# Kernel optimization log

Hardware: AMD Instinct MI355X
Metric: run time of the kernel (lower is better)

Reference implementation:

```python
import jax, jax.numpy as jnp
import numpy as np


def swish(x):
    return x * jax.nn.sigmoid(x)


def setup_inputs() -> dict:
    key = jax.random.key(0)
    ks = jax.random.split(key, 10)
    N, E, R, H = 50000, 300000, 6, 512
    return {
        "x": jax.random.randint(ks[0], (N,), 0, 95),
        "rbf": jax.random.normal(ks[1], (E, R), dtype=jnp.float32),
        "i": jax.random.randint(ks[2], (E,), 0, N),
        "j": jax.random.randint(ks[3], (E,), 0, N),
        "emb_weight": jax.random.normal(ks[4], (95, H), dtype=jnp.float32),
        "W_rbf0": jax.random.normal(ks[5], (R, H), dtype=jnp.float32) * 0.1,
        "b_rbf0": jax.random.normal(ks[6], (H,), dtype=jnp.float32) * 0.1,
        "W_lin": jax.random.normal(ks[7], (3 * H, H), dtype=jnp.float32) * 0.02,
        "b_lin": jax.random.normal(ks[8], (H,), dtype=jnp.float32) * 0.1,
        "W_rbf1": jax.random.normal(ks[9], (R, H), dtype=jnp.float32) * 0.1,
    }


def reference(x, rbf, i, j, emb_weight, W_rbf0, b_rbf0, W_lin, b_lin, W_rbf1):
    # node embedding lookup: [N, H]
    h = emb_weight[x]
    # radial basis projection + swish: [E, H]
    rbf0 = swish(rbf @ W_rbf0 + b_rbf0)
    # gather endpoints, concat, linear, swish: [E, H]
    cat = jnp.concatenate([h[i], h[j], rbf0], axis=-1)  # [E, 3H]
    e1 = swish(cat @ W_lin + b_lin)
    # bias-free rbf projection, elementwise product: [E, H]
    e2 = (rbf @ W_rbf1) * e1
    return (e1, e2)
```

## Files before the change

### kernel.cpp

```cpp
#include <hip/hip_runtime.h>
#include <hip/hip_bf16.h>

typedef __attribute__((ext_vector_type(8))) short short8;
typedef __attribute__((ext_vector_type(4))) float f32x4;

#define NQ 95
#define HDIM 512
#define RBF 6
#define BM 64

static __device__ __forceinline__ unsigned short f2bf(float f){
  unsigned u = __float_as_uint(f);
  u += 0x7FFF + ((u >> 16) & 1);
  return (unsigned short)(u >> 16);
}
static __device__ __forceinline__ float swishf(float z){
  float e = __expf(-z);
  return z * __builtin_amdgcn_rcpf(1.0f + e);
}

__global__ __launch_bounds__(256) void prep_tables(
    const float* __restrict__ emb, const float* __restrict__ W_lin,
    const float* __restrict__ b_lin, float* __restrict__ P0,
    float* __restrict__ P1)
{
  __shared__ float sE[HDIM];
  const int v   = blockIdx.x % NQ;
  const int tab = blockIdx.x / NQ;
  const int t   = threadIdx.x;
  sE[t]       = emb[v*HDIM + t];
  sE[t + 256] = emb[v*HDIM + t + 256];
  __syncthreads();
  const float* W = W_lin + (size_t)tab * HDIM * HDIM;
  float a0 = tab ? 0.f : b_lin[t];
  float a1 = tab ? 0.f : b_lin[t + 256];
  #pragma unroll 4
  for (int k = 0; k < HDIM; ++k){
    float ew = sE[k];
    a0 += ew * W[(size_t)k*HDIM + t];
    a1 += ew * W[(size_t)k*HDIM + t + 256];
  }
  float* P = tab ? P1 : P0;
  P[v*HDIM + t]       = a0;
  P[v*HDIM + t + 256] = a1;
}

__global__ __launch_bounds__(256) void prep_w2t(
    const float* __restrict__ W_lin, unsigned short* __restrict__ W2T)
{
  const int idx = blockIdx.x * 256 + threadIdx.x;
  const int n  = idx >> 6;
  const int kb = (idx & 63) * 8;
  const float* W2 = W_lin + (size_t)1024 * HDIM;
  unsigned p[4];
  #pragma unroll
  for (int c = 0; c < 4; ++c){
    unsigned lo = f2bf(W2[(size_t)(kb + 2*c    ) * HDIM + n]);
    unsigned hi = f2bf(W2[(size_t)(kb + 2*c + 1) * HDIM + n]);
    p[c] = lo | (hi << 16);
  }
  uint4 o; o.x = p[0]; o.y = p[1]; o.z = p[2]; o.w = p[3];
  *(uint4*)(W2T + (size_t)n * HDIM + kb) = o;
}

__global__ __launch_bounds__(512, 4) void fused_edge(
    const int* __restrict__ xv, const float* __restrict__ rbf,
    const int* __restrict__ ei, const int* __restrict__ ej,
    const float* __restrict__ W0, const float* __restrict__ b0,
    const float* __restrict__ W1,
    const float* __restrict__ P0, const float* __restrict__ P1,
    const unsigned short* __restrict__ W2T,
    float* __restrict__ out, int E)
{
  __shared__ unsigned short sA[BM * HDIM];
  __shared__ float sRbf[BM * RBF];
  __shared__ int sXi[BM], sXj[BM];

  const int t  = threadIdx.x;
  const int eb = blockIdx.x * BM;
  const int me = min(BM, E - eb);

  if (t < 96){
    float4 v = make_float4(0.f, 0.f, 0.f, 0.f);
    size_t gi  = (size_t)eb * RBF + (size_t)t * 4;
    size_t lim = (size_t)E * RBF;
    if (gi + 4 <= lim) v = *(const float4*)(rbf + gi);
    else {
      float* pv = (float*)&v;
      for (int c = 0; c < 4; ++c) if (gi + c < lim) pv[c] = rbf[gi + c];
    }
    *(float4*)(sRbf + t*4) = v;
  } else if (t >= 128 && t < 192){
    int q = t - 128;
    int xi = 0, xj = 0;
    int e = eb + q;
    if (e < E){ xi = xv[ei[e]]; xj = xv[ej[e]]; }
    sXi[q] = xi; sXj[q] = xj;
  }

  const int cp   = t & 255;
  const int half = t >> 8;
  float2 w0c[RBF];
  #pragma unroll
  for (int r = 0; r < RBF; ++r) w0c[r] = *(const float2*)(W0 + r*HDIM + 2*cp);
  float2 bb = *(const float2*)(b0 + 2*cp);

  __syncthreads();

  char* sAb = (char*)sA;
  {
    const int swz_t = 4 * cp;
    const int m0 = half * 32;
    #pragma unroll 2
    for (int mm = 0; mm < 32; ++mm){
      const int m = m0 + mm;
      float2 ra = *(const float2*)(sRbf + m*RBF);
      float2 rb = *(const float2*)(sRbf + m*RBF + 2);
      float2 rc = *(const float2*)(sRbf + m*RBF + 4);
      float z0 = bb.x, z1 = bb.y;
      z0 += ra.x*w0c[0].x + ra.y*w0c[1].x + rb.x*w0c[2].x
          + rb.y*w0c[3].x + rc.x*w0c[4].x + rc.y*w0c[5].x;
      z1 += ra.x*w0c[0].y + ra.y*w0c[1].y + rb.x*w0c[2].y
          + rb.y*w0c[3].y + rc.x*w0c[4].y + rc.y*w0c[5].y;
      unsigned pk = (unsigned)f2bf(swishf(z0)) | ((unsigned)f2bf(swishf(z1)) << 16);
      *(unsigned*)(sAb + (m*1024 + (swz_t ^ ((m & 7) << 4)))) = pk;
    }
  }
  __syncthreads();

  const int lane  = t & 63;
  const int w     = t >> 6;
  const int nbase = w * 64;
  const int rlo   = lane & 15;
  const int kg    = lane >> 4;

  f32x4 acc[4][4];
  #pragma unroll
  for (int a = 0; a < 4; ++a)
    #pragma unroll
    for (int b = 0; b < 4; ++b) acc[a][b] = f32x4{0.f, 0.f, 0.f, 0.f};

  for (int ks = 0; ks < 16; ++ks){
    short8 af[4];
    #pragma unroll
    for (int mt = 0; mt < 4; ++mt){
      int row = mt*16 + rlo;
      int off = row*1024 + ((ks*64 + kg*16) ^ ((row & 7) << 4));
      af[mt] = *(const short8*)(sAb + off);
    }
    short8 bfr[4];
    #pragma unroll
    for (int nt = 0; nt < 4; ++nt){
      int n = nbase + nt*16 + rlo;
      bfr[nt] = *(const short8*)(W2T + (size_t)n*HDIM + ks*32 + kg*8);
    }
    #pragma unroll
    for (int nt = 0; nt < 4; ++nt)
      #pragma unroll
      for (int mt = 0; mt < 4; ++mt)
        acc[mt][nt] = __builtin_amdgcn_mfma_f32_16x16x32_bf16(af[mt], bfr[nt], acc[mt][nt], 0, 0, 0);
  }

  float w1c[RBF][4];
  #pragma unroll
  for (int nt = 0; nt < 4; ++nt){
    int n = nbase + nt*16 + rlo;
    #pragma unroll
    for (int r = 0; r < RBF; ++r) w1c[r][nt] = W1[r*HDIM + n];
  }

  float* __restrict__ out2 = out + (size_t)E * HDIM;
  #pragma unroll
  for (int mt = 0; mt < 4; ++mt){
    #pragma unroll
    for (int r = 0; r < 4; ++r){
      const int m  = mt*16 + kg*4 + r;
      const bool valid = (m < me);
      const int xi = sXi[m], xj = sXj[m];
      const float* p0row = P0 + (size_t)xi * HDIM;
      const float* p1row = P1 + (size_t)xj * HDIM;
      const size_t orow = (size_t)(eb + m) * HDIM;
      float2 rra = *(const float2*)(sRbf + m*RBF);
      float2 rrb = *(const float2*)(sRbf + m*RBF + 2);
      float2 rrc = *(const float2*)(sRbf + m*RBF + 4);
      #pragma unroll
      for (int nt = 0; nt < 4; ++nt){
        const int n = nbase + nt*16 + rlo;
        float f  = acc[mt][nt][r] + p0row[n] + p1row[n];
        float e1 = swishf(f);
        float g  = rra.x*w1c[0][nt] + rra.y*w1c[1][nt] + rrb.x*w1c[2][nt]
                 + rrb.y*w1c[3][nt] + rrc.x*w1c[4][nt] + rrc.y*w1c[5][nt];
        if (valid){
          __builtin_nontemporal_store(e1,    out  + orow + n);
          __builtin_nontemporal_store(g*e1,  out2 + orow + n);
        }
      }
    }
  }
}

extern "C" void kernel_launch(void* const* d_in, const int* in_sizes, int n_in,
                              void* d_out, int out_size, void* d_ws, size_t ws_size,
                              hipStream_t stream) {
  const int*   xv    = (const int*)  d_in[0];
  const float* rbf   = (const float*)d_in[1];
  const int*   ei    = (const int*)  d_in[2];
  const int*   ej    = (const int*)  d_in[3];
  const float* emb   = (const float*)d_in[4];
  const float* W0    = (const float*)d_in[5];
  const float* b0    = (const float*)d_in[6];
  const float* W_lin = (const float*)d_in[7];
  const float* b_lin = (const float*)d_in[8];
  const float* W1    = (const float*)d_in[9];
  float* out = (float*)d_out;

  const int E = in_sizes[2];

  float* P0 = (float*)d_ws;
  float* P1 = P0 + NQ * HDIM;
  unsigned short* W2T = (unsigned short*)(P1 + NQ * HDIM);

  prep_tables<<<2 * NQ, 256, 0, stream>>>(emb, W_lin, b_lin, P0, P1);
  prep_w2t<<<(HDIM * (HDIM/8)) / 256, 256, 0, stream>>>(W_lin, W2T);

  const int nblk = (E + BM - 1) / BM;
  fused_edge<<<nblk, 512, 0, stream>>>(xv, rbf, ei, ej, W0, b0, W1,
                                       P0, P1, W2T, out, E);
}
```

Before: 537.4 us.

## Double thread count per block in fused edge and prep kernels

The fused edge kernel now launches 1024 threads (16 waves) per 64-edge block, and each wave owns 32 output columns instead of 64. Per-wave accumulators drop from 16 to 8 tiles, the B-fragment pointers are hoisted, and the k-loop is unrolled. The rbf projection prologue is split four ways. prep_tables moves to 512 threads with one output column per thread. The aim is more waves in flight to hide global-memory latency on the gathers and stores, at the cost of more LDS A-fragment reads per MFMA and possibly lower occupancy per CU given the 64KB of shared memory.

New measurement: 572.9 us. 6.6% more time.

```diff
diff --git a/kernel.cpp b/kernel.cpp
--- a/kernel.cpp
+++ b/kernel.cpp
@@ -19,7 +19,7 @@
   return z * __builtin_amdgcn_rcpf(1.0f + e);
 }
 
-__global__ __launch_bounds__(256) void prep_tables(
+__global__ __launch_bounds__(512) void prep_tables(
     const float* __restrict__ emb, const float* __restrict__ W_lin,
     const float* __restrict__ b_lin, float* __restrict__ P0,
     float* __restrict__ P1)
@@ -28,21 +28,14 @@
   const int v   = blockIdx.x % NQ;
   const int tab = blockIdx.x / NQ;
   const int t   = threadIdx.x;
-  sE[t]       = emb[v*HDIM + t];
-  sE[t + 256] = emb[v*HDIM + t + 256];
+  sE[t] = emb[v*HDIM + t];
   __syncthreads();
-  const float* W = W_lin + (size_t)tab * HDIM * HDIM;
-  float a0 = tab ? 0.f : b_lin[t];
-  float a1 = tab ? 0.f : b_lin[t + 256];
-  #pragma unroll 4
-  for (int k = 0; k < HDIM; ++k){
-    float ew = sE[k];
-    a0 += ew * W[(size_t)k*HDIM + t];
-    a1 += ew * W[(size_t)k*HDIM + t + 256];
-  }
-  float* P = tab ? P1 : P0;
-  P[v*HDIM + t]       = a0;
-  P[v*HDIM + t + 256] = a1;
+  const float* W = W_lin + (size_t)tab * HDIM * HDIM + t;
+  float a = tab ? 0.f : b_lin[t];
+  #pragma unroll 8
+  for (int k = 0; k < HDIM; ++k)
+    a += sE[k] * W[(size_t)k * HDIM];
+  (tab ? P1 : P0)[v*HDIM + t] = a;
 }
 
 __global__ __launch_bounds__(256) void prep_w2t(
@@ -63,7 +56,7 @@
   *(uint4*)(W2T + (size_t)n * HDIM + kb) = o;
 }
 
-__global__ __launch_bounds__(512, 4) void fused_edge(
+__global__ __launch_bounds__(1024, 4) void fused_edge(
     const int* __restrict__ xv, const float* __restrict__ rbf,
     const int* __restrict__ ei, const int* __restrict__ ej,
     const float* __restrict__ W0, const float* __restrict__ b0,
@@ -98,8 +91,8 @@
     sXi[q] = xi; sXj[q] = xj;
   }
 
-  const int cp   = t & 255;
-  const int half = t >> 8;
+  const int cp = t & 255;
+  const int q4 = t >> 8;
   float2 w0c[RBF];
   #pragma unroll
   for (int r = 0; r < RBF; ++r) w0c[r] = *(const float2*)(W0 + r*HDIM + 2*cp);
@@ -110,9 +103,9 @@
   char* sAb = (char*)sA;
   {
     const int swz_t = 4 * cp;
-    const int m0 = half * 32;
+    const int m0 = q4 * 16;
     #pragma unroll 2
-    for (int mm = 0; mm < 32; ++mm){
+    for (int mm = 0; mm < 16; ++mm){
       const int m = m0 + mm;
       float2 ra = *(const float2*)(sRbf + m*RBF);
       float2 rb = *(const float2*)(sRbf + m*RBF + 2);
@@ -130,17 +123,23 @@
 
   const int lane  = t & 63;
   const int w     = t >> 6;
-  const int nbase = w * 64;
+  const int nbase = w * 32;
   const int rlo   = lane & 15;
   const int kg    = lane >> 4;
 
-  f32x4 acc[4][4];
+  f32x4 acc[4][2];
   #pragma unroll
   for (int a = 0; a < 4; ++a)
     #pragma unroll
-    for (int b = 0; b < 4; ++b) acc[a][b] = f32x4{0.f, 0.f, 0.f, 0.f};
-
+    for (int b = 0; b < 2; ++b) acc[a][b] = f32x4{0.f, 0.f, 0.f, 0.f};
+
+  const unsigned short* bp0 = W2T + (size_t)(nbase      + rlo)*HDIM + kg*8;
+  const unsigned short* bp1 = bp0 + (size_t)16*HDIM;
+
+  #pragma unroll 4
   for (int ks = 0; ks < 16; ++ks){
+    short8 b0r = *(const short8*)(bp0 + ks*32);
+    short8 b1r = *(const short8*)(bp1 + ks*32);
     short8 af[4];
     #pragma unroll
     for (int mt = 0; mt < 4; ++mt){
@@ -148,22 +147,16 @@
       int off = row*1024 + ((ks*64 + kg*16) ^ ((row & 7) << 4));
       af[mt] = *(const short8*)(sAb + off);
     }
-    short8 bfr[4];
-    #pragma unroll
-    for (int nt = 0; nt < 4; ++nt){
-      int n = nbase + nt*16 + rlo;
-      bfr[nt] = *(const short8*)(W2T + (size_t)n*HDIM + ks*32 + kg*8);
-    }
-    #pragma unroll
-    for (int nt = 0; nt < 4; ++nt)
-      #pragma unroll
-      for (int mt = 0; mt < 4; ++mt)
-        acc[mt][nt] = __builtin_amdgcn_mfma_f32_16x16x32_bf16(af[mt], bfr[nt], acc[mt][nt], 0, 0, 0);
-  }
-
-  float w1c[RBF][4];
-  #pragma unroll
-  for (int nt = 0; nt < 4; ++nt){
+    #pragma unroll
+    for (int mt = 0; mt < 4; ++mt){
+      acc[mt][0] = __builtin_amdgcn_mfma_f32_16x16x32_bf16(af[mt], b0r, acc[mt][0], 0, 0, 0);
+      acc[mt][1] = __builtin_amdgcn_mfma_f32_16x16x32_bf16(af[mt], b1r, acc[mt][1], 0, 0, 0);
+    }
+  }
+
+  float w1c[RBF][2];
+  #pragma unroll
+  for (int nt = 0; nt < 2; ++nt){
     int n = nbase + nt*16 + rlo;
     #pragma unroll
     for (int r = 0; r < RBF; ++r) w1c[r][nt] = W1[r*HDIM + n];
@@ -180,19 +173,19 @@
       const float* p0row = P0 + (size_t)xi * HDIM;
       const float* p1row = P1 + (size_t)xj * HDIM;
       const size_t orow = (size_t)(eb + m) * HDIM;
-      float2 rra = *(const float2*)(sRbf + m*RBF);
-      float2 rrb = *(const float2*)(sRbf + m*RBF + 2);
-      float2 rrc = *(const float2*)(sRbf + m*RBF + 4);
+      float2 ra = *(const float2*)(sRbf + m*RBF);
+      float2 rb = *(const float2*)(sRbf + m*RBF + 2);
+      float2 rc = *(const float2*)(sRbf + m*RBF + 4);
       #pragma unroll
-      for (int nt = 0; nt < 4; ++nt){
+      for (int nt = 0; nt < 2; ++nt){
         const int n = nbase + nt*16 + rlo;
         float f  = acc[mt][nt][r] + p0row[n] + p1row[n];
         float e1 = swishf(f);
-        float g  = rra.x*w1c[0][nt] + rra.y*w1c[1][nt] + rrb.x*w1c[2][nt]
-                 + rrb.y*w1c[3][nt] + rrc.x*w1c[4][nt] + rrc.y*w1c[5][nt];
+        float g  = ra.x*w1c[0][nt] + ra.y*w1c[1][nt] + rb.x*w1c[2][nt]
+                 + rb.y*w1c[3][nt] + rc.x*w1c[4][nt] + rc.y*w1c[5][nt];
         if (valid){
-          __builtin_nontemporal_store(e1,    out  + orow + n);
-          __builtin_nontemporal_store(g*e1,  out2 + orow + n);
+          __builtin_nontemporal_store(e1,   out  + orow + n);
+          __builtin_nontemporal_store(g*e1, out2 + orow + n);
         }
       }
     }
@@ -220,10 +213,10 @@
   float* P1 = P0 + NQ * HDIM;
   unsigned short* W2T = (unsigned short*)(P1 + NQ * HDIM);
 
-  prep_tables<<<2 * NQ, 256, 0, stream>>>(emb, W_lin, b_lin, P0, P1);
+  prep_tables<<<2 * NQ, 512, 0, stream>>>(emb, W_lin, b_lin, P0, P1);
   prep_w2t<<<(HDIM * (HDIM/8)) / 256, 256, 0, stream>>>(W_lin, W2T);
 
   const int nblk = (E + BM - 1) / BM;
-  fused_edge<<<nblk, 512, 0, stream>>>(xv, rbf, ei, ej, W0, b0, W1,
-                                       P0, P1, W2T, out, E);
-}
+  fused_edge<<<nblk, 1024, 0, stream>>>(xv, rbf, ei, ej, W0, b0, W1,
+                                        P0, P1, W2T, out, E);
+}
```
